# Performance work log

Hardware: AMD Instinct MI355X
Metric: run time of the kernel (lower is better)

The kernel has to match this reference:

```python
import jax, jax.numpy as jnp
import numpy as np

N_NODES = 50000
N_EDGES = 800000
HID = 256
HEADS = 4
HEAD_C = HID // HEADS  # 64
IN_CH = 16
OUT_CH = 4
NEG_SLOPE = 0.2  # PyG GATConv default LeakyReLU slope
LN_EPS = 1e-5


def setup_inputs() -> dict:
    key = jax.random.key(0)
    ks = jax.random.split(key, 12)
    s = 0.05
    return {
        "x": jax.random.normal(ks[0], (N_NODES, IN_CH), dtype=jnp.float32),
        "edge_index": jax.random.randint(ks[1], (2, N_EDGES), 0, N_NODES, dtype=jnp.int64),
        "w_in": jax.random.normal(ks[2], (IN_CH, HID), dtype=jnp.float32) * s,
        "b_in": jnp.zeros((HID,), dtype=jnp.float32),
        "w_gat": jax.random.normal(ks[3], (4, HID, HID), dtype=jnp.float32) * s,
        "att_src": jax.random.normal(ks[4], (4, HEADS, HEAD_C), dtype=jnp.float32) * s,
        "att_dst": jax.random.normal(ks[5], (4, HEADS, HEAD_C), dtype=jnp.float32) * s,
        "b_gat": jnp.zeros((4, HID), dtype=jnp.float32),
        "ln_scale": jnp.ones((4, HID), dtype=jnp.float32),
        "ln_bias": jnp.zeros((4, HID), dtype=jnp.float32),
        "w_out": jax.random.normal(ks[6], (HID, OUT_CH), dtype=jnp.float32) * s,
        "b_out": jnp.zeros((OUT_CH,), dtype=jnp.float32),
    }


def _gat_layer(x, src, dst, W, a_src, a_dst, bias, g, beta):
    """One GATConv(concat, heads=4) + LayerNorm + ELU. x:[N,HID]."""
    n = x.shape[0]
    h = (x @ W).reshape(n, HEADS, HEAD_C)                 # [N,H,C]
    a_s = jnp.einsum("nhc,hc->nh", h, a_src)              # [N,H]
    a_d = jnp.einsum("nhc,hc->nh", h, a_dst)              # [N,H]
    logits = jax.nn.leaky_relu(a_s[src] + a_d[dst], NEG_SLOPE)  # [E,H]
    # segment softmax over destination neighborhoods (self-loops ensure non-empty)
    m = jax.ops.segment_max(logits, dst, num_segments=n)
    e = jnp.exp(logits - m[dst])
    denom = jax.ops.segment_sum(e, dst, num_segments=n)
    alpha = e / (denom[dst] + 1e-16)                      # [E,H]
    msg = alpha[:, :, None] * h[src]                      # [E,H,C]
    out = jax.ops.segment_sum(msg, dst, num_segments=n).reshape(n, HID) + bias
    mu = out.mean(-1, keepdims=True)
    var = out.var(-1, keepdims=True)
    out = (out - mu) * jax.lax.rsqrt(var + LN_EPS) * g + beta
    return jax.nn.elu(out)


def reference(x, edge_index, w_in, b_in, w_gat, att_src, att_dst, b_gat,
              ln_scale, ln_bias, w_out, b_out):
    n = x.shape[0]
    # PyG GATConv adds self-loops by default
    loops = jnp.arange(n, dtype=edge_index.dtype)
    ei = jnp.concatenate([edge_index, jnp.stack([loops, loops])], axis=1)
    src, dst = ei[0], ei[1]

    x = x @ w_in + b_in                                   # input_proj
    h = x
    for l in (0, 1):
        h = _gat_layer(h, src, dst, w_gat[l], att_src[l], att_dst[l],
                       b_gat[l], ln_scale[l], ln_bias[l])
    x = x + h
    h = x
    for l in (2, 3):
        h = _gat_layer(h, src, dst, w_gat[l], att_src[l], att_dst[l],
                       b_gat[l], ln_scale[l], ln_bias[l])
    x = x + h
    return x @ w_out + b_out
```

## Files before the change

### kernel.cpp

```cpp
#include <hip/hip_runtime.h>
#include <math.h>

#define NN 50000
#define E0 800000
#define ET 850000
#define HID 256
#define INCH 16
#define MAXDEG 64

#define NB_Z    49
#define NB_WT   256
#define NB_IP   6250
#define NB_PREP (NB_Z + NB_WT + NB_IP)

#define NB_G    782
#define EPB     2048
#define NB_SC   416
#define NB_G0   (NB_SC + NB_G)

typedef _Float16 h8 __attribute__((ext_vector_type(8)));
typedef float f32x4 __attribute__((ext_vector_type(4)));

__device__ __forceinline__ void load_lds16(const void* g, void* l) {
    __builtin_amdgcn_global_load_lds(
        (const __attribute__((address_space(1))) unsigned int*)g,
        (__attribute__((address_space(3))) unsigned int*)l, 16, 0, 0);
}

__global__ __launch_bounds__(256) void prep_kernel(
    int* __restrict__ cursor,
    const float* __restrict__ w_gat, _Float16* __restrict__ WT,
    const float* __restrict__ x, const float* __restrict__ w_in,
    const float* __restrict__ b_in, _Float16* __restrict__ Ph) {
    int b = blockIdx.x, t = threadIdx.x;
    if (b < NB_Z) {
        int i = (b * 256 + t) * 4;
#pragma unroll
        for (int k = 0; k < 4; ++k)
            if (i + k < NN) cursor[i + k] = 0;
    } else if (b < NB_Z + NB_WT) {
        int k = b - NB_Z;
#pragma unroll
        for (int l = 0; l < 4; ++l) {
            float v = w_gat[((size_t)l * 256 + k) * 256 + t];
            WT[((size_t)l * 256 + t) * 256 + k] = (_Float16)v;
        }
    } else {
        int ipb = b - NB_Z - NB_WT;
        int sub = t >> 5, l32 = t & 31;
        int n = ipb * 8 + sub;
        int c0 = l32 * 8;
        const float* xr = x + n * INCH;
        float a[8];
#pragma unroll
        for (int k = 0; k < 8; k += 4) {
            float4 bb = *(const float4*)(b_in + c0 + k);
            a[k] = bb.x; a[k + 1] = bb.y; a[k + 2] = bb.z; a[k + 3] = bb.w;
        }
#pragma unroll
        for (int k = 0; k < INCH; ++k) {
            float xv = xr[k];
            const float4 w0 = *(const float4*)(w_in + k * 256 + c0);
            const float4 w1 = *(const float4*)(w_in + k * 256 + c0 + 4);
            a[0] += xv * w0.x; a[1] += xv * w0.y; a[2] += xv * w0.z; a[3] += xv * w0.w;
            a[4] += xv * w1.x; a[5] += xv * w1.y; a[6] += xv * w1.z; a[7] += xv * w1.w;
        }
        h8 o;
#pragma unroll
        for (int k = 0; k < 8; ++k) o[k] = (_Float16)a[k];
        *(h8*)(Ph + (size_t)n * 256 + c0) = o;
    }
}

__device__ __forceinline__ void gemm_tile(
    int rb, int cb,
    const _Float16* __restrict__ A, const _Float16* __restrict__ BT,
    _Float16* __restrict__ H, const float* __restrict__ att_s,
    const float* __restrict__ att_d, float* __restrict__ AS, float* __restrict__ AD,
    _Float16* As, _Float16* Bs) {
    int t = threadIdx.x;
    int wv = t >> 6, lane = t & 63;
    int wr = (wv >> 1) * 64, wc = (wv & 1) * 64;
    int lm = lane & 15, lq = lane >> 4;
    f32x4 acc[4][4] = {};

    int rch = lane >> 2;
    int q = lane & 3;

    for (int k0 = 0; k0 < 256; k0 += 32) {
#pragma unroll
        for (int c = 0; c < 2; ++c) {
            int r = wv * 32 + c * 16 + rch;
            int g = q ^ (r & 3);
            int ra = rb + r; if (ra >= NN) ra = NN - 1;
            load_lds16(A + (size_t)ra * 256 + k0 + g * 8,
                       (char*)As + wv * 2048 + c * 1024);
            load_lds16(BT + (size_t)(cb + r) * 256 + k0 + g * 8,
                       (char*)Bs + wv * 2048 + c * 1024);
        }
        __syncthreads();
        h8 af[4], bfr[4];
#pragma unroll
        for (int i = 0; i < 4; ++i) {
            int row = wr + i * 16 + lm;
            af[i] = *(const h8*)((const char*)As + row * 64 + ((lq ^ (row & 3)) * 16));
        }
#pragma unroll
        for (int j = 0; j < 4; ++j) {
            int row = wc + j * 16 + lm;
            bfr[j] = *(const h8*)((const char*)Bs + row * 64 + ((lq ^ (row & 3)) * 16));
        }
#pragma unroll
        for (int i = 0; i < 4; ++i)
#pragma unroll
            for (int j = 0; j < 4; ++j)
                acc[i][j] = __builtin_amdgcn_mfma_f32_16x16x32_f16(af[i], bfr[j], acc[i][j], 0, 0, 0);
        __syncthreads();
    }

    int head = (cb + wc) >> 6;
    float sa[4], sd[4];
#pragma unroll
    for (int j = 0; j < 4; ++j) {
        sa[j] = att_s[head * 64 + j * 16 + lm];
        sd[j] = att_d[head * 64 + j * 16 + lm];
    }
#pragma unroll
    for (int i = 0; i < 4; ++i)
#pragma unroll
        for (int rr = 0; rr < 4; ++rr) {
            float vs = acc[i][0][rr] * sa[0] + acc[i][1][rr] * sa[1]
                     + acc[i][2][rr] * sa[2] + acc[i][3][rr] * sa[3];
            float vd = acc[i][0][rr] * sd[0] + acc[i][1][rr] * sd[1]
                     + acc[i][2][rr] * sd[2] + acc[i][3][rr] * sd[3];
#pragma unroll
            for (int o = 1; o <= 8; o <<= 1) {
                vs += __shfl_xor(vs, o, 64);
                vd += __shfl_xor(vd, o, 64);
            }
            int row = rb + wr + i * 16 + lq * 4 + rr;
            if (lm == 0 && row < NN) {
                AS[row * 4 + head] = vs;
                AD[row * 4 + head] = vd;
            }
        }

#pragma unroll
    for (int i = 0; i < 4; ++i)
#pragma unroll
        for (int j = 0; j < 4; ++j) {
            int col = cb + wc + j * 16 + lm;
#pragma unroll
            for (int rr = 0; rr < 4; ++rr) {
                int row = rb + wr + i * 16 + lq * 4 + rr;
                if (row < NN) H[(size_t)row * 256 + col] = (_Float16)acc[i][j][rr];
            }
        }
}

__global__ __launch_bounds__(256) void gemm_fused_kernel(
    const _Float16* __restrict__ A, const _Float16* __restrict__ BT,
    _Float16* __restrict__ H, const float* __restrict__ att_s,
    const float* __restrict__ att_d, float* __restrict__ AS, float* __restrict__ AD) {
    __shared__ _Float16 As[128 * 32];
    __shared__ _Float16 Bs[128 * 32];
    gemm_tile(blockIdx.x * 128, blockIdx.y * 128, A, BT, H, att_s, att_d, AS, AD, As, Bs);
}

__global__ __launch_bounds__(256) void gemm0_scatter_kernel(
    const _Float16* __restrict__ A, const _Float16* __restrict__ BT,
    _Float16* __restrict__ H, const float* __restrict__ att_s,
    const float* __restrict__ att_d, float* __restrict__ AS, float* __restrict__ AD,
    const int* __restrict__ ei, int* __restrict__ cursor, int* __restrict__ csr_pad) {
    __shared__ _Float16 As[128 * 32];
    __shared__ _Float16 Bs[128 * 32];
    int b = blockIdx.x;
    if (b < NB_SC) {
        int base = b * EPB + threadIdx.x;
#pragma unroll
        for (int k = 0; k < 8; ++k) {
            int e = base + k * 256;
            if (e < ET) {
                int s, d;
                if (e < E0) { s = ei[e]; d = ei[E0 + e]; }
                else        { s = d = e - E0; }
                int pos = atomicAdd(&cursor[d], 1);
                if (pos < MAXDEG) csr_pad[(d << 6) + pos] = s;
            }
        }
        return;
    }
    int g = b - NB_SC;
    gemm_tile((g >> 1) * 128, (g & 1) * 128, A, BT, H, att_s, att_d, AS, AD, As, Bs);
}

__global__ __launch_bounds__(256) void agg_kernel(
    const _Float16* __restrict__ H, const float4* __restrict__ AS,
    const float4* __restrict__ AD,
    const int* __restrict__ cnt, const int* __restrict__ csr_pad,
    const float* __restrict__ bias, const float* __restrict__ g, const float* __restrict__ beta,
    const _Float16* __restrict__ res, _Float16* __restrict__ outh,
    const float* __restrict__ wout, const float* __restrict__ bout,
    float* __restrict__ out) {
    int t = threadIdx.x;
    int l32 = t & 31;
    int n = blockIdx.x * 8 + (t >> 5);
    int deg = cnt[n];
    if (deg > MAXDEG) deg = MAXDEG;
    int start = n << 6, end = start + deg;
    float4 adv = AD[n];
    int head = l32 >> 3;
    int c0 = l32 * 8;
    float advh = (head == 0) ? adv.x : (head == 1) ? adv.y : (head == 2) ? adv.z : adv.w;

    float acc[8] = {};
    float acc_e = 0.f;
#pragma unroll 4
    for (int i = start; i < end; ++i) {
        int s = csr_pad[i];
        const float* as = (const float*)&AS[s];
        float v = as[head] + advh;
        v = (v >= 0.f) ? v : 0.2f * v;
        float e = __expf(v);
        acc_e += e;
        h8 hv = *(const h8*)(H + (size_t)s * 256 + c0);
#pragma unroll
        for (int k = 0; k < 8; ++k) acc[k] += e * (float)hv[k];
    }
    float dinv = 1.f / (acc_e + 1e-16f);

    float val[8];
#pragma unroll
    for (int k = 0; k < 8; k += 4) {
        float4 bb = *(const float4*)(bias + c0 + k);
        val[k]     = acc[k]     * dinv + bb.x;
        val[k + 1] = acc[k + 1] * dinv + bb.y;
        val[k + 2] = acc[k + 2] * dinv + bb.z;
        val[k + 3] = acc[k + 3] * dinv + bb.w;
    }

    float s1 = 0.f, s2 = 0.f;
#pragma unroll
    for (int k = 0; k < 8; ++k) { s1 += val[k]; s2 += val[k] * val[k]; }
#pragma unroll
    for (int o = 16; o >= 1; o >>= 1) {
        s1 += __shfl_xor(s1, o, 64);
        s2 += __shfl_xor(s2, o, 64);
    }
    float mu = s1 * (1.f / 256.f);
    float var = s2 * (1.f / 256.f) - mu * mu;
    float rs = rsqrtf(var + 1e-5f);

    float y[8];
#pragma unroll
    for (int k = 0; k < 8; k += 4) {
        float4 g4 = *(const float4*)(g + c0 + k);
        float4 b4 = *(const float4*)(beta + c0 + k);
        y[k]     = (val[k]     - mu) * rs * g4.x + b4.x;
        y[k + 1] = (val[k + 1] - mu) * rs * g4.y + b4.y;
        y[k + 2] = (val[k + 2] - mu) * rs * g4.z + b4.z;
        y[k + 3] = (val[k + 3] - mu) * rs * g4.w + b4.w;
    }
#pragma unroll
    for (int k = 0; k < 8; ++k) y[k] = (y[k] > 0.f) ? y[k] : (__expf(y[k]) - 1.f);
    if (res) {
        h8 r0 = *(const h8*)(res + (size_t)n * 256 + c0);
#pragma unroll
        for (int k = 0; k < 8; ++k) y[k] += (float)r0[k];
    }
    if (wout) {
        float o0 = 0.f, o1 = 0.f, o2 = 0.f, o3 = 0.f;
#pragma unroll
        for (int k = 0; k < 8; ++k) {
            float4 wv = *(const float4*)(wout + (size_t)(c0 + k) * 4);
            o0 += y[k] * wv.x; o1 += y[k] * wv.y; o2 += y[k] * wv.z; o3 += y[k] * wv.w;
        }
#pragma unroll
        for (int o = 16; o >= 1; o >>= 1) {
            o0 += __shfl_xor(o0, o, 64);
            o1 += __shfl_xor(o1, o, 64);
            o2 += __shfl_xor(o2, o, 64);
            o3 += __shfl_xor(o3, o, 64);
        }
        if (l32 == 0) {
            float4 ov = make_float4(o0 + bout[0], o1 + bout[1], o2 + bout[2], o3 + bout[3]);
            *(float4*)(out + (size_t)n * 4) = ov;
        }
    } else {
        h8 o0;
#pragma unroll
        for (int k = 0; k < 8; ++k) o0[k] = (_Float16)y[k];
        *(h8*)(outh + (size_t)n * 256 + c0) = o0;
    }
}

extern "C" void kernel_launch(void* const* d_in, const int* in_sizes, int n_in,
                              void* d_out, int out_size, void* d_ws, size_t ws_size,
                              hipStream_t stream) {
    const float* x       = (const float*)d_in[0];
    const int*   ei      = (const int*)  d_in[1];
    const float* w_in    = (const float*)d_in[2];
    const float* b_in    = (const float*)d_in[3];
    const float* w_gat   = (const float*)d_in[4];
    const float* att_src = (const float*)d_in[5];
    const float* att_dst = (const float*)d_in[6];
    const float* b_gat   = (const float*)d_in[7];
    const float* ln_g    = (const float*)d_in[8];
    const float* ln_b    = (const float*)d_in[9];
    const float* w_out   = (const float*)d_in[10];
    const float* b_out   = (const float*)d_in[11];
    float* out = (float*)d_out;

    char* ws = (char*)d_ws;
    size_t off = 0;
    auto alloc = [&](size_t bytes) {
        void* p = ws + off;
        off += (bytes + 255) & ~(size_t)255;
        return p;
    };
    _Float16*  Ph      = (_Float16*)alloc((size_t)NN * HID * 2);
    _Float16*  Ch      = (_Float16*)alloc((size_t)NN * HID * 2);
    _Float16*  Gh      = (_Float16*)alloc((size_t)NN * HID * 2);
    _Float16*  H       = (_Float16*)alloc((size_t)NN * HID * 2);
    _Float16*  WT      = (_Float16*)alloc((size_t)4 * HID * HID * 2);
    float*     ASAD    = (float*)alloc((size_t)NN * 8 * 4);
    int*       cursor  = (int*)alloc((size_t)NN * 4);
    int*       csr_pad = (int*)alloc((size_t)NN * MAXDEG * 4);

    float* AS = ASAD;
    float* AD = ASAD + (size_t)NN * 4;

    const dim3 GEMM_GRID(391, 2);
    const int NB_AGG = NN / 8;

    prep_kernel<<<NB_PREP, 256, 0, stream>>>(cursor, w_gat, WT, x, w_in, b_in, Ph);

    gemm0_scatter_kernel<<<NB_G0, 256, 0, stream>>>(
        Ph, WT, H, att_src, att_dst, AS, AD, ei, cursor, csr_pad);
    agg_kernel<<<NB_AGG, 256, 0, stream>>>(
        H, (const float4*)AS, (const float4*)AD, cursor, csr_pad,
        b_gat, ln_g, ln_b, nullptr, Gh, nullptr, nullptr, nullptr);

    auto run_layer = [&](const _Float16* inh, int l, const _Float16* res, _Float16* outh,
                         const float* wo, const float* bo) {
        gemm_fused_kernel<<<GEMM_GRID, 256, 0, stream>>>(
            inh, WT + (size_t)l * HID * HID, H,
            att_src + l * 256, att_dst + l * 256, AS, AD);
        agg_kernel<<<NB_AGG, 256, 0, stream>>>(
            H, (const float4*)AS, (const float4*)AD, cursor, csr_pad,
            b_gat + l * 256, ln_g + l * 256, ln_b + l * 256, res, outh, wo, bo,
            wo ? out : nullptr);
    };

    run_layer(Gh, 1, Ph,      Ch, nullptr, nullptr);
    run_layer(Ch, 2, nullptr, Gh, nullptr, nullptr);
    run_layer(Gh, 3, Ch,      Ph, w_out,   b_out);
}
```

Before: 528.9 us.

## Replace global-atomic CSR build with two-pass bucketed sort and 16-bit indices

```diff
diff --git a/kernel.cpp b/kernel.cpp
--- a/kernel.cpp
+++ b/kernel.cpp
@@ -8,15 +8,16 @@
 #define INCH 16
 #define MAXDEG 64
 
-#define NB_Z    49
+#define NB_P1   416
+#define EPB     2048
+#define NBUCK   196
+
 #define NB_WT   256
 #define NB_IP   6250
-#define NB_PREP (NB_Z + NB_WT + NB_IP)
+#define NB_PREP (NB_P1 + NB_WT + NB_IP)
 
 #define NB_G    782
-#define EPB     2048
-#define NB_SC   416
-#define NB_G0   (NB_SC + NB_G)
+#define NB_G0   (NBUCK + NB_G)
 
 typedef _Float16 h8 __attribute__((ext_vector_type(8)));
 typedef float f32x4 __attribute__((ext_vector_type(4)));
@@ -28,25 +29,65 @@
 }
 
 __global__ __launch_bounds__(256) void prep_kernel(
-    int* __restrict__ cursor,
     const float* __restrict__ w_gat, _Float16* __restrict__ WT,
     const float* __restrict__ x, const float* __restrict__ w_in,
-    const float* __restrict__ b_in, _Float16* __restrict__ Ph) {
+    const float* __restrict__ b_in, _Float16* __restrict__ Ph,
+    const int* __restrict__ ei, unsigned int* __restrict__ pairs,
+    int* __restrict__ cnt_g, int* __restrict__ off_g) {
+    __shared__ unsigned int hist[256], pref[256], cur2[256];
     int b = blockIdx.x, t = threadIdx.x;
-    if (b < NB_Z) {
-        int i = (b * 256 + t) * 4;
-#pragma unroll
-        for (int k = 0; k < 4; ++k)
-            if (i + k < NN) cursor[i + k] = 0;
-    } else if (b < NB_Z + NB_WT) {
-        int k = b - NB_Z;
+    if (b < NB_P1) {
+        hist[t] = 0;
+        __syncthreads();
+        unsigned int pk[8];
+        int base = b * EPB + t;
+#pragma unroll
+        for (int k = 0; k < 8; ++k) {
+            int e = base + k * 256;
+            pk[k] = 0xFFFFFFFFu;
+            if (e < ET) {
+                int s, d;
+                if (e < E0) { s = ei[e]; d = ei[E0 + e]; }
+                else        { s = d = e - E0; }
+                pk[k] = ((unsigned int)d << 16) | (unsigned int)s;
+                atomicAdd(&hist[d >> 8], 1u);
+            }
+        }
+        __syncthreads();
+        unsigned int h = hist[t];
+        pref[t] = h;
+        __syncthreads();
+#pragma unroll
+        for (int o = 1; o < 256; o <<= 1) {
+            unsigned int v = (t >= o) ? pref[t - o] : 0u;
+            __syncthreads();
+            pref[t] += v;
+            __syncthreads();
+        }
+        unsigned int ex = pref[t] - h;
+        cur2[t] = ex;
+        if (t < NBUCK) {
+            cnt_g[b * NBUCK + t] = (int)h;
+            off_g[b * NBUCK + t] = (int)ex;
+        }
+        __syncthreads();
+#pragma unroll
+        for (int k = 0; k < 8; ++k) {
+            if (pk[k] != 0xFFFFFFFFu) {
+                unsigned int g = pk[k] >> 24;
+                unsigned int pos = atomicAdd(&cur2[g], 1u);
+                pairs[b * EPB + pos] = pk[k];
+            }
+        }
+    } else if (b < NB_P1 + NB_WT) {
+        int k = b - NB_P1;
 #pragma unroll
         for (int l = 0; l < 4; ++l) {
             float v = w_gat[((size_t)l * 256 + k) * 256 + t];
             WT[((size_t)l * 256 + t) * 256 + k] = (_Float16)v;
         }
     } else {
-        int ipb = b - NB_Z - NB_WT;
+        int ipb = b - NB_P1 - NB_WT;
         int sub = t >> 5, l32 = t & 31;
         int n = ipb * 8 + sub;
         int c0 = l32 * 8;
@@ -167,37 +208,46 @@
     gemm_tile(blockIdx.x * 128, blockIdx.y * 128, A, BT, H, att_s, att_d, AS, AD, As, Bs);
 }
 
-__global__ __launch_bounds__(256) void gemm0_scatter_kernel(
+__global__ __launch_bounds__(256) void gemm0_p2_kernel(
     const _Float16* __restrict__ A, const _Float16* __restrict__ BT,
     _Float16* __restrict__ H, const float* __restrict__ att_s,
     const float* __restrict__ att_d, float* __restrict__ AS, float* __restrict__ AD,
-    const int* __restrict__ ei, int* __restrict__ cursor, int* __restrict__ csr_pad) {
+    const unsigned int* __restrict__ pairs, const int* __restrict__ cnt_g,
+    const int* __restrict__ off_g, int* __restrict__ cursor,
+    unsigned short* __restrict__ csr_pad) {
     __shared__ _Float16 As[128 * 32];
     __shared__ _Float16 Bs[128 * 32];
     int b = blockIdx.x;
-    if (b < NB_SC) {
-        int base = b * EPB + threadIdx.x;
-#pragma unroll
-        for (int k = 0; k < 8; ++k) {
-            int e = base + k * 256;
-            if (e < ET) {
-                int s, d;
-                if (e < E0) { s = ei[e]; d = ei[E0 + e]; }
-                else        { s = d = e - E0; }
-                int pos = atomicAdd(&cursor[d], 1);
-                if (pos < MAXDEG) csr_pad[(d << 6) + pos] = s;
-            }
-        }
+    if (b < NBUCK) {
+        int g = b, t = threadIdx.x;
+        unsigned int* curs = (unsigned int*)As;
+        curs[t] = 0;
+        __syncthreads();
+        for (int sb = t; sb < NB_P1; sb += 256) {
+            int c = cnt_g[sb * NBUCK + g];
+            int o = off_g[sb * NBUCK + g];
+            const unsigned int* p = pairs + sb * EPB + o;
+            for (int i = 0; i < c; ++i) {
+                unsigned int pk = p[i];
+                int d = (int)(pk >> 16);
+                unsigned int pos = atomicAdd(&curs[d & 255], 1u);
+                if (pos < MAXDEG)
+                    csr_pad[((size_t)d << 6) + pos] = (unsigned short)(pk & 0xFFFFu);
+            }
+        }
+        __syncthreads();
+        int n = (g << 8) + t;
+        if (n < NN) cursor[n] = (int)curs[t];
         return;
     }
-    int g = b - NB_SC;
-    gemm_tile((g >> 1) * 128, (g & 1) * 128, A, BT, H, att_s, att_d, AS, AD, As, Bs);
+    int g2 = b - NBUCK;
+    gemm_tile((g2 >> 1) * 128, (g2 & 1) * 128, A, BT, H, att_s, att_d, AS, AD, As, Bs);
 }
 
 __global__ __launch_bounds__(256) void agg_kernel(
     const _Float16* __restrict__ H, const float4* __restrict__ AS,
     const float4* __restrict__ AD,
-    const int* __restrict__ cnt, const int* __restrict__ csr_pad,
+    const int* __restrict__ cnt, const unsigned short* __restrict__ csr_pad,
     const float* __restrict__ bias, const float* __restrict__ g, const float* __restrict__ beta,
     const _Float16* __restrict__ res, _Float16* __restrict__ outh,
     const float* __restrict__ wout, const float* __restrict__ bout,
@@ -318,14 +368,17 @@
         off += (bytes + 255) & ~(size_t)255;
         return p;
     };
-    _Float16*  Ph      = (_Float16*)alloc((size_t)NN * HID * 2);
-    _Float16*  Ch      = (_Float16*)alloc((size_t)NN * HID * 2);
-    _Float16*  Gh      = (_Float16*)alloc((size_t)NN * HID * 2);
-    _Float16*  H       = (_Float16*)alloc((size_t)NN * HID * 2);
-    _Float16*  WT      = (_Float16*)alloc((size_t)4 * HID * HID * 2);
-    float*     ASAD    = (float*)alloc((size_t)NN * 8 * 4);
-    int*       cursor  = (int*)alloc((size_t)NN * 4);
-    int*       csr_pad = (int*)alloc((size_t)NN * MAXDEG * 4);
+    _Float16*       Ph      = (_Float16*)alloc((size_t)NN * HID * 2);
+    _Float16*       Ch      = (_Float16*)alloc((size_t)NN * HID * 2);
+    _Float16*       Gh      = (_Float16*)alloc((size_t)NN * HID * 2);
+    _Float16*       H       = (_Float16*)alloc((size_t)NN * HID * 2);
+    _Float16*       WT      = (_Float16*)alloc((size_t)4 * HID * HID * 2);
+    float*          ASAD    = (float*)alloc((size_t)NN * 8 * 4);
+    int*            cursor  = (int*)alloc((size_t)NN * 4);
+    unsigned short* csr_pad = (unsigned short*)alloc((size_t)NN * MAXDEG * 2);
+    unsigned int*   pairs   = (unsigned int*)alloc((size_t)NB_P1 * EPB * 4);
+    int*            cnt_g   = (int*)alloc((size_t)NB_P1 * NBUCK * 4);
+    int*            off_g   = (int*)alloc((size_t)NB_P1 * NBUCK * 4);
 
     float* AS = ASAD;
     float* AD = ASAD + (size_t)NN * 4;
@@ -333,10 +386,11 @@
     const dim3 GEMM_GRID(391, 2);
     const int NB_AGG = NN / 8;
 
-    prep_kernel<<<NB_PREP, 256, 0, stream>>>(cursor, w_gat, WT, x, w_in, b_in, Ph);
-
-    gemm0_scatter_kernel<<<NB_G0, 256, 0, stream>>>(
-        Ph, WT, H, att_src, att_dst, AS, AD, ei, cursor, csr_pad);
+    prep_kernel<<<NB_PREP, 256, 0, stream>>>(w_gat, WT, x, w_in, b_in, Ph,
+                                             ei, pairs, cnt_g, off_g);
+
+    gemm0_p2_kernel<<<NB_G0, 256, 0, stream>>>(
+        Ph, WT, H, att_src, att_dst, AS, AD, pairs, cnt_g, off_g, cursor, csr_pad);
     agg_kernel<<<NB_AGG, 256, 0, stream>>>(
         H, (const float4*)AS, (const float4*)AD, cursor, csr_pad,
         b_gat, ln_g, ln_b, nullptr, Gh, nullptr, nullptr, nullptr);
```

After: 527.7 us. About the same (-0.2%).
